# Kernel optimization log

Hardware: AMD Instinct MI355X
Metric: run time of the kernel (lower is better)

The kernel has to match this reference:

```python
import jax, jax.numpy as jnp
import numpy as np

NZ, NX, NY = 128, 256, 256
N_GAUSS = 50000
SIGMA_CUTOFF = 3.0
R = 3  # hardcoded stencil radius in voxelize()


def setup_inputs() -> dict:
    key = jax.random.key(0)
    k1, k2, k3, k4 = jax.random.split(key, 4)
    centers = jax.random.uniform(k1, (N_GAUSS, 3), jnp.float32) * 2.0 - 1.0
    log_scales = jnp.full((N_GAUSS, 3), -4.0, jnp.float32)
    rho_real = jax.random.normal(k2, (N_GAUSS,), jnp.float32) * 0.1
    rho_imag = jax.random.normal(k3, (N_GAUSS,), jnp.float32) * 0.1
    # k-space undersampling mask (0/1)
    mask = (jax.random.uniform(k4, (NZ, NX, NY), jnp.float32) < 0.3).astype(jnp.float32)
    return {"mask": mask, "centers": centers, "log_scales": log_scales,
            "rho_real": rho_real, "rho_imag": rho_imag}


def _voxelize(centers, log_scales, rho_real, rho_imag):
    gr = jnp.arange(-R, R + 1)
    kz, kx, ky = jnp.meshgrid(gr, gr, gr, indexing='ij')
    offsets = jnp.stack([kz, kx, ky], axis=-1).reshape(-1, 3)  # [K,3], K=343
    dims = jnp.array([NZ, NX, NY], jnp.int32)
    gsm1 = (dims - 1).astype(jnp.float32)  # grid_size - 1
    # nearest voxel of each gaussian center ([-1,1] -> grid coords)
    ci = jnp.round((centers + 1.0) * 0.5 * gsm1).astype(jnp.int32)  # [M,3]
    ni = ci[:, None, :] + offsets[None, :, :]                        # [M,K,3]
    in_bounds = jnp.all((ni >= 0) & (ni < dims), axis=-1)            # [M,K]
    # neighbor coords back in normalized [-1,1] space
    nc = ni.astype(jnp.float32) / gsm1 * 2.0 - 1.0                   # [M,K,3]
    scales = jnp.exp(log_scales)
    delta = (nc - centers[:, None, :]) / (scales[:, None, :] + 1e-8)
    dist_sq = jnp.sum(delta * delta, axis=-1)                        # [M,K]
    valid = in_bounds & (dist_sq <= SIGMA_CUTOFF ** 2)
    w = jnp.where(valid, jnp.exp(-0.5 * dist_sq), 0.0)               # [M,K]
    vals_r = (rho_real[:, None] * w).ravel()
    vals_i = (rho_imag[:, None] * w).ravel()
    # clip indices for safety; invalid entries contribute 0
    nic = jnp.clip(ni, 0, dims - 1)
    flat = ((nic[..., 0] * NX + nic[..., 1]) * NY + nic[..., 2]).ravel()
    vol_r = jnp.zeros(NZ * NX * NY, jnp.float32).at[flat].add(vals_r).reshape(NZ, NX, NY)
    vol_i = jnp.zeros(NZ * NX * NY, jnp.float32).at[flat].add(vals_i).reshape(NZ, NX, NY)
    return vol_r + 1j * vol_i


def _image_to_kspace(vol):
    # centered orthonormal 3D FFT (standard MRI convention)
    return jnp.fft.fftshift(jnp.fft.fftn(jnp.fft.ifftshift(vol), norm='ortho'))


def reference(mask, centers, log_scales, rho_real, rho_imag):
    volume = _voxelize(centers, log_scales, rho_real, rho_imag)
    kspace_pred = mask * _image_to_kspace(volume)
    return (volume, kspace_pred)
```

## Files before the change

### kernel.cpp

```cpp
#include <hip/hip_runtime.h>
#include <math.h>

#define NZd 128
#define NXd 256
#define NYd 256
#define NVOX (NZd * NXd * NYd)
#define PI_F 3.14159265358979323846f
#define SCALE_ORTHO 3.4526698300124393e-4f
#define CAP 512

__global__ void zero_kernel(float4* __restrict__ p, int n4) {
    int i = blockIdx.x * blockDim.x + threadIdx.x;
    if (i < n4) p[i] = make_float4(0.f, 0.f, 0.f, 0.f);
}
__global__ void zero_ints_kernel(int* __restrict__ p, int n) {
    int i = blockIdx.x * blockDim.x + threadIdx.x;
    if (i < n) p[i] = 0;
}

__global__ void voxelize_kernel(const float* __restrict__ centers,
                                const float* __restrict__ log_scales,
                                const float* __restrict__ rho_r,
                                const float* __restrict__ rho_i,
                                float* __restrict__ vol, int M) {
    long long t = (long long)blockIdx.x * blockDim.x + threadIdx.x;
    if (t >= (long long)M * 343) return;
    int g = (int)(t / 343);
    int k = (int)(t % 343);
    int oz = k / 49 - 3, ox = (k / 7) % 7 - 3, oy = k % 7 - 3;
    float cz = centers[g * 3 + 0], cx = centers[g * 3 + 1], cy = centers[g * 3 + 2];
    int iz = (int)rintf((cz + 1.0f) * 0.5f * 127.0f);
    int ix = (int)rintf((cx + 1.0f) * 0.5f * 255.0f);
    int iy = (int)rintf((cy + 1.0f) * 0.5f * 255.0f);
    int nz = iz + oz, nx = ix + ox, ny = iy + oy;
    if (nz < 0 || nz >= NZd || nx < 0 || nx >= NXd || ny < 0 || ny >= NYd) return;
    float sz = expf(log_scales[g * 3 + 0]) + 1e-8f;
    float sx = expf(log_scales[g * 3 + 1]) + 1e-8f;
    float sy = expf(log_scales[g * 3 + 2]) + 1e-8f;
    float dz = ((float)nz / 127.0f * 2.0f - 1.0f - cz) / sz;
    float dx = ((float)nx / 255.0f * 2.0f - 1.0f - cx) / sx;
    float dy = ((float)ny / 255.0f * 2.0f - 1.0f - cy) / sy;
    float d2 = dz * dz + dx * dx + dy * dy;
    if (d2 > 9.0f) return;
    float w = expf(-0.5f * d2);
    int idx = (nz * NXd + nx) * NYd + ny;
    atomicAdd(&vol[2 * idx + 0], rho_r[g] * w);
    atomicAdd(&vol[2 * idx + 1], rho_i[g] * w);
}

__global__ void copy_real_kernel(const float2* __restrict__ cvol,
                                 float* __restrict__ out) {
    int i = blockIdx.x * blockDim.x + threadIdx.x;
    out[i] = cvol[i].x;
}

__device__ __forceinline__ void center_voxel(const float* __restrict__ centers,
                                             int g, int& iz, int& ix, int& iy) {
    float cz = centers[g * 3 + 0], cx = centers[g * 3 + 1], cy = centers[g * 3 + 2];
    iz = min(max((int)rintf((cz + 1.0f) * 0.5f * 127.0f), 0), 127);
    ix = min(max((int)rintf((cx + 1.0f) * 0.5f * 255.0f), 0), 255);
    iy = min(max((int)rintf((cy + 1.0f) * 0.5f * 255.0f), 0), 255);
}

__global__ void bin_count_kernel(const float* __restrict__ centers,
                                 int* __restrict__ cnt, int M) {
    int g = blockIdx.x * blockDim.x + threadIdx.x;
    if (g >= M) return;
    int iz, ix, iy;
    center_voxel(centers, g, iz, ix, iy);
    atomicAdd(&cnt[((iz >> 4) << 8) | ((ix >> 4) << 4) | (iy >> 4)], 1);
}

__global__ void bin_scan_kernel(const int* __restrict__ cnt,
                                int* __restrict__ off,
                                int* __restrict__ cursor) {
    int lane = threadIdx.x;
    int base = lane << 5;
    int s = 0;
    #pragma unroll
    for (int i = 0; i < 32; i++) s += cnt[base + i];
    int incl = s;
    #pragma unroll
    for (int d = 1; d < 64; d <<= 1) {
        int v = __shfl_up(incl, d, 64);
        if (lane >= d) incl += v;
    }
    int run = incl - s;
    for (int i = 0; i < 32; i++) {
        int c = cnt[base + i];
        off[base + i] = run;
        cursor[base + i] = run;
        run += c;
    }
}

__global__ void bin_scatter_kernel(const float* __restrict__ centers,
                                   const float* __restrict__ log_scales,
                                   const float* __restrict__ rho_r,
                                   const float* __restrict__ rho_i,
                                   int* __restrict__ cursor,
                                   int* __restrict__ ciA,
                                   float* __restrict__ czA, float* __restrict__ cxA,
                                   float* __restrict__ cyA,
                                   float* __restrict__ iszA, float* __restrict__ isxA,
                                   float* __restrict__ isyA,
                                   float* __restrict__ rrA, float* __restrict__ riA,
                                   int M) {
    int g = blockIdx.x * blockDim.x + threadIdx.x;
    if (g >= M) return;
    int iz, ix, iy;
    center_voxel(centers, g, iz, ix, iy);
    int b = ((iz >> 4) << 8) | ((ix >> 4) << 4) | (iy >> 4);
    int pos = atomicAdd(&cursor[b], 1);
    ciA[pos] = (iz << 16) | (ix << 8) | iy;
    czA[pos] = centers[g * 3 + 0];
    cxA[pos] = centers[g * 3 + 1];
    cyA[pos] = centers[g * 3 + 2];
    iszA[pos] = 1.0f / (expf(log_scales[g * 3 + 0]) + 1e-8f);
    isxA[pos] = 1.0f / (expf(log_scales[g * 3 + 1]) + 1e-8f);
    isyA[pos] = 1.0f / (expf(log_scales[g * 3 + 2]) + 1e-8f);
    rrA[pos] = rho_r[g];
    riA[pos] = rho_i[g];
}

__global__ __launch_bounds__(256) void tile_accum_kernel(
        const int* __restrict__ cnt, const int* __restrict__ off,
        const int* __restrict__ ciA,
        const float* __restrict__ czA, const float* __restrict__ cxA,
        const float* __restrict__ cyA,
        const float* __restrict__ iszA, const float* __restrict__ isxA,
        const float* __restrict__ isyA,
        const float* __restrict__ rrA, const float* __restrict__ riA,
        float2* __restrict__ cvol, float* __restrict__ out_vr) {
    __shared__ int   sci[CAP];
    __shared__ float scz[CAP], scx[CAP], scy[CAP];
    __shared__ float sisz[CAP], sisx[CAP], sisy[CAP];
    __shared__ float srr[CAP], sri[CAP];
    __shared__ int wcnt[4];

    int tile = blockIdx.x;
    int ty = tile & 15, tx = (tile >> 4) & 15, tz = tile >> 8;
    int z0 = tz << 3, x0 = tx << 4, y0 = ty << 4;
    int t = threadIdx.x;
    int lane = t & 63, wid = t >> 6;
    int yl = t & 15, xl = t >> 4;
    int nx = x0 + xl, ny = y0 + yl;
    float nxf = (float)nx * (2.0f / 255.0f) - 1.0f;
    float nyf = (float)ny * (2.0f / 255.0f) - 1.0f;

    float accR[8], accI[8], zfs[8];
    #pragma unroll
    for (int i = 0; i < 8; i++) {
        accR[i] = 0.f; accI[i] = 0.f;
        zfs[i] = (float)(z0 + i) * (2.0f / 127.0f) - 1.0f;
    }

    int bzl = max(z0 - 3, 0) >> 4,  bzh = min(z0 + 10, 127) >> 4;
    int bxl = max(x0 - 3, 0) >> 4,  bxh = min(x0 + 18, 255) >> 4;
    int byl = max(y0 - 3, 0) >> 4,  byh = min(y0 + 18, 255) >> 4;

#define MKRANGE(slot, BZ, BX, VALID)                                          \
    int qs##slot = 0, len##slot = 0;                                          \
    if (VALID) {                                                              \
        int bl_ = ((BZ) << 8) | ((BX) << 4) | byl;                            \
        int bh_ = ((BZ) << 8) | ((BX) << 4) | byh;                            \
        qs##slot = off[bl_];                                                  \
        len##slot = off[bh_] + cnt[bh_] - qs##slot;                           \
    }
    bool hz1 = (bzh > bzl);
    bool hx1 = (bxh >= bxl + 1), hx2 = (bxh >= bxl + 2);
    MKRANGE(0, bzl,     bxl,     true)
    MKRANGE(1, bzl,     bxl + 1, hx1)
    MKRANGE(2, bzl,     bxl + 2, hx2)
    MKRANGE(3, bzl + 1, bxl,     hz1)
    MKRANGE(4, bzl + 1, bxl + 1, hz1 && hx1)
    MKRANGE(5, bzl + 1, bxl + 2, hz1 && hx2)
#undef MKRANGE
    int cum1 = len0;
    int cum2 = cum1 + len1;
    int cum3 = cum2 + len2;
    int cum4 = cum3 + len3;
    int cum5 = cum4 + len4;
    int T    = cum5 + len5;

    int lc = 0;
    for (int f0 = 0; f0 < T; f0 += 256) {
        int f = f0 + t;
        bool keep = false;
        int cpv = 0;
        float czv, cxv, cyv, iszv, isxv, isyv, rrv, riv;
        if (f < T) {
            int q = qs0 + f;
            if (f >= cum1) q = qs1 + (f - cum1);
            if (f >= cum2) q = qs2 + (f - cum2);
            if (f >= cum3) q = qs3 + (f - cum3);
            if (f >= cum4) q = qs4 + (f - cum4);
            if (f >= cum5) q = qs5 + (f - cum5);
            cpv = ciA[q];
            int iz = cpv >> 16, ix = (cpv >> 8) & 255, iy = cpv & 255;
            keep = !(ix + 3 < x0 || ix > x0 + 18 ||
                     iy + 3 < y0 || iy > y0 + 18 ||
                     iz + 3 < z0 || iz > z0 + 10);
            if (keep) {
                czv = czA[q]; cxv = cxA[q]; cyv = cyA[q];
                iszv = iszA[q]; isxv = isxA[q]; isyv = isyA[q];
                rrv = rrA[q]; riv = riA[q];
            }
        }
        unsigned long long m = __ballot(keep);
        __syncthreads();
        if (lane == 0) wcnt[wid] = __popcll(m);
        __syncthreads();
        int ntot = wcnt[0] + wcnt[1] + wcnt[2] + wcnt[3];
        if (lc + ntot > CAP) {
            for (int u = 0; u < lc; u++) {
                int cp = sci[u];
                int iz = cp >> 16, ix = (cp >> 8) & 255, iy = cp & 255;
                int dxi = nx - ix, dyi = ny - iy;
                if (dxi < -3 || dxi > 3 || dyi < -3 || dyi > 3) continue;
                float dxv = (nxf - scx[u]) * sisx[u];
                float dyv = (nyf - scy[u]) * sisy[u];
                float dxy2 = dxv * dxv + dyv * dyv;
                if (dxy2 > 9.0f) continue;
                float cz_ = scz[u], isz_ = sisz[u];
                float rr = srr[u], ri = sri[u];
                int zlo = max(z0, iz - 3) - z0;
                int zhi = min(z0 + 7, iz + 3) - z0;
                #pragma unroll
                for (int zl = 0; zl < 8; zl++) {
                    if (zl >= zlo && zl <= zhi) {
                        float dzv = (zfs[zl] - cz_) * isz_;
                        float d2 = dxy2 + dzv * dzv;
                        if (d2 <= 9.0f) {
                            float w = __expf(-0.5f * d2);
                            accR[zl] += rr * w;
                            accI[zl] += ri * w;
                        }
                    }
                }
            }
            __syncthreads();
            lc = 0;
        }
        int basew = lc;
        #pragma unroll
        for (int w = 0; w < 4; w++) if (w < wid) basew += wcnt[w];
        if (keep) {
            int pos = basew + __popcll(m & ((1ULL << lane) - 1));
            sci[pos] = cpv;
            scz[pos] = czv; scx[pos] = cxv; scy[pos] = cyv;
            sisz[pos] = iszv; sisx[pos] = isxv; sisy[pos] = isyv;
            srr[pos] = rrv; sri[pos] = riv;
        }
        lc += ntot;
    }
    __syncthreads();
    for (int u = 0; u < lc; u++) {
        int cp = sci[u];
        int iz = cp >> 16, ix = (cp >> 8) & 255, iy = cp & 255;
        int dxi = nx - ix, dyi = ny - iy;
        if (dxi < -3 || dxi > 3 || dyi < -3 || dyi > 3) continue;
        float dxv = (nxf - scx[u]) * sisx[u];
        float dyv = (nyf - scy[u]) * sisy[u];
        float dxy2 = dxv * dxv + dyv * dyv;
        if (dxy2 > 9.0f) continue;
        float cz_ = scz[u], isz_ = sisz[u];
        float rr = srr[u], ri = sri[u];
        int zlo = max(z0, iz - 3) - z0;
        int zhi = min(z0 + 7, iz + 3) - z0;
        #pragma unroll
        for (int zl = 0; zl < 8; zl++) {
            if (zl >= zlo && zl <= zhi) {
                float dzv = (zfs[zl] - cz_) * isz_;
                float d2 = dxy2 + dzv * dzv;
                if (d2 <= 9.0f) {
                    float w = __expf(-0.5f * d2);
                    accR[zl] += rr * w;
                    accI[zl] += ri * w;
                }
            }
        }
    }

    #pragma unroll
    for (int zl = 0; zl < 8; zl++) {
        size_t idx = ((size_t)(z0 + zl) * NXd + nx) * NYd + ny;
        cvol[idx] = make_float2(accR[zl], accI[zl]);
        out_vr[idx] = accR[zl];
    }
}

template <int L>
__device__ __forceinline__ void fft_lds(float2* buf) {
    int tid = threadIdx.x;
    for (int half = 1; half < L; half <<= 1) {
        __syncthreads();
        int j = tid & (half - 1);
        int i0 = ((tid ^ j) << 1) | j;
        int i1 = i0 + half;
        float ang = -PI_F * (float)j / (float)half;
        float s, c;
        sincosf(ang, &s, &c);
        float2 a = buf[i0];
        float2 b = buf[i1];
        float tr = c * b.x - s * b.y;
        float ti = c * b.y + s * b.x;
        buf[i0] = make_float2(a.x + tr, a.y + ti);
        buf[i1] = make_float2(a.x - tr, a.y - ti);
    }
    __syncthreads();
}

__global__ void fft_y_kernel(const float2* __restrict__ src,
                             float2* __restrict__ dst) {
    __shared__ float2 buf[256];
    __shared__ float2 tw[128];
    int l = blockIdx.x;
    int tid = threadIdx.x;
    {
        float s, c;
        sincosf(-PI_F * (float)tid / 128.0f, &s, &c);
        tw[tid] = make_float2(c, s);
    }
    int p = ((l >> 8) + l) & 1;
    const float2* s = src + (size_t)l * NYd;
    for (int i = tid; i < 256; i += 128) {
        float2 v = s[i];
        if ((p + i) & 1) { v.x = -v.x; v.y = -v.y; }
        buf[__brev((unsigned)i) >> 24] = v;
    }
    #pragma unroll
    for (int st = 0; st < 8; st++) {
        const int half = 1 << st;
        const int twstep = 128 >> st;
        __syncthreads();
        int j = tid & (half - 1);
        int i0 = ((tid ^ j) << 1) | j;
        int i1 = i0 + half;
        float2 w = tw[j * twstep];
        float2 a = buf[i0];
        float2 b = buf[i1];
        float tr = w.x * b.x - w.y * b.y;
        float ti = w.x * b.y + w.y * b.x;
        buf[i0] = make_float2(a.x + tr, a.y + ti);
        buf[i1] = make_float2(a.x - tr, a.y - ti);
    }
    __syncthreads();
    float2* d = dst + (size_t)l * NYd;
    for (int i = tid; i < 256; i += 128) d[i] = buf[i];
}

__global__ void fft_x_kernel(float2* __restrict__ ks) {
    __shared__ float2 buf[256];
    int l = blockIdx.x;
    int tid = threadIdx.x;
    int z = l >> 8, y = l & 255;
    float2* base = ks + (size_t)z * (NXd * NYd) + y;
    for (int i = tid; i < 256; i += 128)
        buf[__brev((unsigned)i) >> 24] = base[(size_t)i * NYd];
    fft_lds<256>(buf);
    for (int i = tid; i < 256; i += 128)
        base[(size_t)i * NYd] = buf[i];
}
__global__ void fft_z_kernel(float2* __restrict__ ks,
                             const float* __restrict__ mask,
                             float* __restrict__ out_real) {
    __shared__ float2 buf[128];
    int l = blockIdx.x;
    int tid = threadIdx.x;
    float2* base = ks + l;
    for (int i = tid; i < 128; i += 64)
        buf[__brev((unsigned)i) >> 25] = base[(size_t)i * (NXd * NYd)];
    fft_lds<128>(buf);
    int p = ((l >> 8) + l) & 1;
    for (int i = tid; i < 128; i += 64) {
        float2 v = buf[i];
        float sgn = ((p + i) & 1) ? -SCALE_ORTHO : SCALE_ORTHO;
        float m = mask[(size_t)i * (NXd * NYd) + l] * sgn;
        if (out_real) {
            out_real[(size_t)i * (NXd * NYd) + l] = v.x * m;
        } else {
            v.x *= m; v.y *= m;
            base[(size_t)i * (NXd * NYd)] = v;
        }
    }
}

__global__ __launch_bounds__(256) void fft_x16_kernel(float2* __restrict__ ks) {
    __shared__ float2 buf[16][256 + 1];
    __shared__ float2 tw[128];
    int t = threadIdx.x;
    int blk = blockIdx.x;
    int z = blk >> 4;
    int y16 = (blk & 15) << 4;
    if (t < 128) {
        float s, c;
        sincosf(-PI_F * (float)t / 128.0f, &s, &c);
        tw[t] = make_float2(c, s);
    }
    float2* base = ks + (size_t)z * (NXd * NYd) + y16;
    int yl = t & 15, xe0 = t >> 4;
    #pragma unroll
    for (int p = 0; p < 16; p++) {
        int xe = xe0 + (p << 4);
        float2 v = base[(size_t)xe * NYd + yl];
        buf[yl][__brev((unsigned)xe) >> 24] = v;
    }
    int s_ = t & 127;
    int fb0 = t >> 7;
    #pragma unroll
    for (int st = 0; st < 8; st++) {
        const int half = 1 << st;
        const int twstep = 128 >> st;
        __syncthreads();
        int j = s_ & (half - 1);
        int i0 = ((s_ ^ j) << 1) | j;
        int i1 = i0 + half;
        float2 w = tw[j * twstep];
        #pragma unroll
        for (int u = 0; u < 8; u++) {
            int fb = fb0 + (u << 1);
            float2 a = buf[fb][i0];
            float2 b = buf[fb][i1];
            float tr = w.x * b.x - w.y * b.y;
            float ti = w.x * b.y + w.y * b.x;
            buf[fb][i0] = make_float2(a.x + tr, a.y + ti);
            buf[fb][i1] = make_float2(a.x - tr, a.y - ti);
        }
    }
    __syncthreads();
    #pragma unroll
    for (int p = 0; p < 16; p++) {
        int xe = xe0 + (p << 4);
        base[(size_t)xe * NYd + yl] = buf[yl][xe];
    }
}

__global__ __launch_bounds__(256) void fft_z32_kernel(const float2* __restrict__ ks,
                                                      const float* __restrict__ mask,
                                                      float* __restrict__ out_kr) {
    __shared__ float2 buf[32][128 + 1];
    __shared__ float2 tw[64];
    int t = threadIdx.x;
    int blk = blockIdx.x;
    int kx = blk >> 3;
    int ky32 = (blk & 7) << 5;
    if (t < 64) {
        float s, c;
        sincosf(-PI_F * (float)t / 64.0f, &s, &c);
        tw[t] = make_float2(c, s);
    }
    const float2* base = ks + (size_t)kx * NYd + ky32;
    int kyl = t & 31, ze0 = t >> 5;
    #pragma unroll
    for (int p = 0; p < 16; p++) {
        int ze = ze0 + (p << 3);
        float2 v = base[(size_t)ze * (NXd * NYd) + kyl];
        buf[kyl][__brev((unsigned)ze) >> 25] = v;
    }
    int s_ = t & 63;
    int fb0 = t >> 6;
    #pragma unroll
    for (int st = 0; st < 7; st++) {
        const int half = 1 << st;
        const int twstep = 64 >> st;
        __syncthreads();
        int j = s_ & (half - 1);
        int i0 = ((s_ ^ j) << 1) | j;
        int i1 = i0 + half;
        float2 w = tw[j * twstep];
        #pragma unroll
        for (int u = 0; u < 8; u++) {
            int fb = fb0 + (u << 2);
            float2 a = buf[fb][i0];
            float2 b = buf[fb][i1];
            float tr = w.x * b.x - w.y * b.y;
            float ti = w.x * b.y + w.y * b.x;
            buf[fb][i0] = make_float2(a.x + tr, a.y + ti);
            buf[fb][i1] = make_float2(a.x - tr, a.y - ti);
        }
    }
    __syncthreads();
    int ky = ky32 + kyl;
    #pragma unroll
    for (int p = 0; p < 16; p++) {
        int ze = ze0 + (p << 3);
        float2 v = buf[kyl][ze];
        size_t gi = (size_t)ze * (NXd * NYd) + (size_t)kx * NYd + ky;
        float sgn = ((ze + kx + ky) & 1) ? -SCALE_ORTHO : SCALE_ORTHO;
        out_kr[gi] = v.x * (mask[gi] * sgn);
    }
}

extern "C" void kernel_launch(void* const* d_in, const int* in_sizes, int n_in,
                              void* d_out, int out_size, void* d_ws, size_t ws_size,
                              hipStream_t stream) {
    const float* mask       = (const float*)d_in[0];
    const float* centers    = (const float*)d_in[1];
    const float* log_scales = (const float*)d_in[2];
    const float* rho_r      = (const float*)d_in[3];
    const float* rho_i      = (const float*)d_in[4];
    int M = in_sizes[1] / 3;

    bool inter = (out_size >= 4 * NVOX);
    if (!inter) {
        if (out_size < 2 * NVOX || ws_size < (size_t)NVOX * 8) {
            int z4 = out_size / 4;
            if (z4 > 0)
                zero_kernel<<<(z4 + 255) / 256, 256, 0, stream>>>((float4*)d_out, z4);
            return;
        }
        float* out_vr = (float*)d_out;
        float* out_kr = out_vr + NVOX;
        float2* cvol = (float2*)d_ws;

        int Mpad = (M + 63) & ~63;
        bool fast = (8192 + 9LL * Mpad) <= (long long)NVOX;
        if (fast) {
            int* ibase  = (int*)out_kr;
            int* cnt    = ibase;
            int* off    = ibase + 2048;
            int* cursor = ibase + 4096;
            float* fbase = (float*)(ibase + 8192);
            int*   ciA  = (int*)fbase;
            float* czA  = fbase + 1LL * Mpad;
            float* cxA  = fbase + 2LL * Mpad;
            float* cyA  = fbase + 3LL * Mpad;
            float* iszA = fbase + 4LL * Mpad;
            float* isxA = fbase + 5LL * Mpad;
            float* isyA = fbase + 6LL * Mpad;
            float* rrA  = fbase + 7LL * Mpad;
            float* riA  = fbase + 8LL * Mpad;

            zero_ints_kernel<<<8, 256, 0, stream>>>(cnt, 2048);
            bin_count_kernel<<<(M + 255) / 256, 256, 0, stream>>>(centers, cnt, M);
            bin_scan_kernel<<<1, 64, 0, stream>>>(cnt, off, cursor);
            bin_scatter_kernel<<<(M + 255) / 256, 256, 0, stream>>>(
                centers, log_scales, rho_r, rho_i, cursor,
                ciA, czA, cxA, cyA, iszA, isxA, isyA, rrA, riA, M);
            tile_accum_kernel<<<4096, 256, 0, stream>>>(
                cnt, off, ciA, czA, cxA, cyA, iszA, isxA, isyA, rrA, riA,
                cvol, out_vr);
        } else {
            int n4 = (2 * NVOX) / 4;
            zero_kernel<<<(n4 + 255) / 256, 256, 0, stream>>>((float4*)cvol, n4);
            long long total = (long long)M * 343;
            int vb = (int)((total + 255) / 256);
            voxelize_kernel<<<vb, 256, 0, stream>>>(centers, log_scales, rho_r,
                                                    rho_i, (float*)cvol, M);
            copy_real_kernel<<<NVOX / 256, 256, 0, stream>>>(cvol, out_vr);
        }

        fft_y_kernel<<<NZd * NXd, 128, 0, stream>>>(cvol, cvol);
        fft_x16_kernel<<<NZd * 16, 256, 0, stream>>>(cvol);
        fft_z32_kernel<<<NXd * 8, 256, 0, stream>>>(cvol, mask, out_kr);
    } else {
        float2* cvol = (float2*)d_out;
        float2* cks  = cvol + NVOX;
        int n4 = (2 * NVOX) / 4;
        zero_kernel<<<(n4 + 255) / 256, 256, 0, stream>>>((float4*)cvol, n4);
        long long total = (long long)M * 343;
        int vb = (int)((total + 255) / 256);
        voxelize_kernel<<<vb, 256, 0, stream>>>(centers, log_scales, rho_r,
                                                rho_i, (float*)cvol, M);
        fft_y_kernel<<<NZd * NXd, 128, 0, stream>>>(cvol, cks);
        fft_x_kernel<<<NZd * NYd, 128, 0, stream>>>(cks);
        fft_z_kernel<<<NXd * NYd, 64, 0, stream>>>(cks, mask, nullptr);
    }
}
```

Baseline: 196.9 us.

## Pack tile-accum LDS into float4s, add per-wave x culling, batch FFT-y rows

After: 199.6 us. No clear change (+1.4%).

```diff
diff --git a/kernel.cpp b/kernel.cpp
--- a/kernel.cpp
+++ b/kernel.cpp
@@ -12,10 +12,6 @@
 __global__ void zero_kernel(float4* __restrict__ p, int n4) {
     int i = blockIdx.x * blockDim.x + threadIdx.x;
     if (i < n4) p[i] = make_float4(0.f, 0.f, 0.f, 0.f);
-}
-__global__ void zero_ints_kernel(int* __restrict__ p, int n) {
-    int i = blockIdx.x * blockDim.x + threadIdx.x;
-    if (i < n) p[i] = 0;
 }
 
 __global__ void voxelize_kernel(const float* __restrict__ centers,
@@ -132,10 +128,9 @@
         const float* __restrict__ isyA,
         const float* __restrict__ rrA, const float* __restrict__ riA,
         float2* __restrict__ cvol, float* __restrict__ out_vr) {
-    __shared__ int   sci[CAP];
-    __shared__ float scz[CAP], scx[CAP], scy[CAP];
-    __shared__ float sisz[CAP], sisx[CAP], sisy[CAP];
-    __shared__ float srr[CAP], sri[CAP];
+    __shared__ int    sci[CAP];
+    __shared__ float4 srA[CAP];
+    __shared__ float4 srB[CAP];
     __shared__ int wcnt[4];
 
     int tile = blockIdx.x;
@@ -147,6 +142,8 @@
     int nx = x0 + xl, ny = y0 + yl;
     float nxf = (float)nx * (2.0f / 255.0f) - 1.0f;
     float nyf = (float)ny * (2.0f / 255.0f) - 1.0f;
+    int wxlo = x0 + (wid << 2);
+    int wxhi = wxlo + 3;
 
     float accR[8], accI[8], zfs[8];
     #pragma unroll
@@ -182,6 +179,36 @@
     int cum4 = cum3 + len3;
     int cum5 = cum4 + len4;
     int T    = cum5 + len5;
+
+#define PROCESS_LIST()                                                        \
+    for (int u = 0; u < lc; u++) {                                            \
+        int cp = sci[u];                                                      \
+        int ix = (cp >> 8) & 255;                                             \
+        if (ix + 3 < wxlo || ix - 3 > wxhi) continue;       \
+        int iz = cp >> 16, iy = cp & 255;                                     \
+        int dxi = nx - ix, dyi = ny - iy;                                     \
+        bool colok = (dxi >= -3 && dxi <= 3 && dyi >= -3 && dyi <= 3);        \
+        float4 rA = srA[u];                                                   \
+        float dxv = (nxf - rA.x) * rA.z;                                      \
+        float dyv = (nyf - rA.y) * rA.w;                                      \
+        float dxy2 = dxv * dxv + dyv * dyv;                                   \
+        if (!colok || dxy2 > 9.0f) continue;                                  \
+        float4 rB = srB[u];                                                   \
+        int zlo = max(z0, iz - 3) - z0;                                       \
+        int zhi = min(z0 + 7, iz + 3) - z0;                                   \
+        _Pragma("unroll")                                                     \
+        for (int zl = 0; zl < 8; zl++) {                                      \
+            if (zl >= zlo && zl <= zhi) {                                     \
+                float dzv = (zfs[zl] - rB.x) * rB.y;                          \
+                float d2 = dxy2 + dzv * dzv;                                  \
+                if (d2 <= 9.0f) {                                             \
+                    float w = __expf(-0.5f * d2);                             \
+                    accR[zl] += rB.z * w;                                     \
+                    accI[zl] += rB.w * w;                                     \
+                }                                                             \
+            }                                                                 \
+        }                                                                     \
+    }
 
     int lc = 0;
     for (int f0 = 0; f0 < T; f0 += 256) {
@@ -213,32 +240,7 @@
         __syncthreads();
         int ntot = wcnt[0] + wcnt[1] + wcnt[2] + wcnt[3];
         if (lc + ntot > CAP) {
-            for (int u = 0; u < lc; u++) {
-                int cp = sci[u];
-                int iz = cp >> 16, ix = (cp >> 8) & 255, iy = cp & 255;
-                int dxi = nx - ix, dyi = ny - iy;
-                if (dxi < -3 || dxi > 3 || dyi < -3 || dyi > 3) continue;
-                float dxv = (nxf - scx[u]) * sisx[u];
-                float dyv = (nyf - scy[u]) * sisy[u];
-                float dxy2 = dxv * dxv + dyv * dyv;
-                if (dxy2 > 9.0f) continue;
-                float cz_ = scz[u], isz_ = sisz[u];
-                float rr = srr[u], ri = sri[u];
-                int zlo = max(z0, iz - 3) - z0;
-                int zhi = min(z0 + 7, iz + 3) - z0;
-                #pragma unroll
-                for (int zl = 0; zl < 8; zl++) {
-                    if (zl >= zlo && zl <= zhi) {
-                        float dzv = (zfs[zl] - cz_) * isz_;
-                        float d2 = dxy2 + dzv * dzv;
-                        if (d2 <= 9.0f) {
-                            float w = __expf(-0.5f * d2);
-                            accR[zl] += rr * w;
-                            accI[zl] += ri * w;
-                        }
-                    }
-                }
-            }
+            PROCESS_LIST()
             __syncthreads();
             lc = 0;
         }
@@ -248,39 +250,14 @@
         if (keep) {
             int pos = basew + __popcll(m & ((1ULL << lane) - 1));
             sci[pos] = cpv;
-            scz[pos] = czv; scx[pos] = cxv; scy[pos] = cyv;
-            sisz[pos] = iszv; sisx[pos] = isxv; sisy[pos] = isyv;
-            srr[pos] = rrv; sri[pos] = riv;
+            srA[pos] = make_float4(cxv, cyv, isxv, isyv);
+            srB[pos] = make_float4(czv, iszv, rrv, riv);
         }
         lc += ntot;
     }
     __syncthreads();
-    for (int u = 0; u < lc; u++) {
-        int cp = sci[u];
-        int iz = cp >> 16, ix = (cp >> 8) & 255, iy = cp & 255;
-        int dxi = nx - ix, dyi = ny - iy;
-        if (dxi < -3 || dxi > 3 || dyi < -3 || dyi > 3) continue;
-        float dxv = (nxf - scx[u]) * sisx[u];
-        float dyv = (nyf - scy[u]) * sisy[u];
-        float dxy2 = dxv * dxv + dyv * dyv;
-        if (dxy2 > 9.0f) continue;
-        float cz_ = scz[u], isz_ = sisz[u];
-        float rr = srr[u], ri = sri[u];
-        int zlo = max(z0, iz - 3) - z0;
-        int zhi = min(z0 + 7, iz + 3) - z0;
-        #pragma unroll
-        for (int zl = 0; zl < 8; zl++) {
-            if (zl >= zlo && zl <= zhi) {
-                float dzv = (zfs[zl] - cz_) * isz_;
-                float d2 = dxy2 + dzv * dzv;
-                if (d2 <= 9.0f) {
-                    float w = __expf(-0.5f * d2);
-                    accR[zl] += rr * w;
-                    accI[zl] += ri * w;
-                }
-            }
-        }
-    }
+    PROCESS_LIST()
+#undef PROCESS_LIST
 
     #pragma unroll
     for (int zl = 0; zl < 8; zl++) {
@@ -311,23 +288,25 @@
     __syncthreads();
 }
 
-__global__ void fft_y_kernel(const float2* __restrict__ src,
-                             float2* __restrict__ dst) {
-    __shared__ float2 buf[256];
+__global__ __launch_bounds__(256) void fft_y2_kernel(const float2* __restrict__ src,
+                                                     float2* __restrict__ dst) {
+    __shared__ float2 buf[2][256];
     __shared__ float2 tw[128];
-    int l = blockIdx.x;
-    int tid = threadIdx.x;
-    {
+    int t = threadIdx.x;
+    int li = t >> 7;
+    int tid = t & 127;
+    int l = (blockIdx.x << 1) + li;
+    if (t < 128) {
         float s, c;
-        sincosf(-PI_F * (float)tid / 128.0f, &s, &c);
-        tw[tid] = make_float2(c, s);
+        sincosf(-PI_F * (float)t / 128.0f, &s, &c);
+        tw[t] = make_float2(c, s);
     }
     int p = ((l >> 8) + l) & 1;
     const float2* s = src + (size_t)l * NYd;
     for (int i = tid; i < 256; i += 128) {
         float2 v = s[i];
         if ((p + i) & 1) { v.x = -v.x; v.y = -v.y; }
-        buf[__brev((unsigned)i) >> 24] = v;
+        buf[li][__brev((unsigned)i) >> 24] = v;
     }
     #pragma unroll
     for (int st = 0; st < 8; st++) {
@@ -338,18 +317,34 @@
         int i0 = ((tid ^ j) << 1) | j;
         int i1 = i0 + half;
         float2 w = tw[j * twstep];
-        float2 a = buf[i0];
-        float2 b = buf[i1];
+        float2 a = buf[li][i0];
+        float2 b = buf[li][i1];
         float tr = w.x * b.x - w.y * b.y;
         float ti = w.x * b.y + w.y * b.x;
-        buf[i0] = make_float2(a.x + tr, a.y + ti);
-        buf[i1] = make_float2(a.x - tr, a.y - ti);
+        buf[li][i0] = make_float2(a.x + tr, a.y + ti);
+        buf[li][i1] = make_float2(a.x - tr, a.y - ti);
     }
     __syncthreads();
     float2* d = dst + (size_t)l * NYd;
+    for (int i = tid; i < 256; i += 128) d[i] = buf[li][i];
+}
+
+__global__ void fft_y_kernel(const float2* __restrict__ src,
+                             float2* __restrict__ dst) {
+    __shared__ float2 buf[256];
+    int l = blockIdx.x;
+    int tid = threadIdx.x;
+    int p = ((l >> 8) + l) & 1;
+    const float2* s = src + (size_t)l * NYd;
+    for (int i = tid; i < 256; i += 128) {
+        float2 v = s[i];
+        if ((p + i) & 1) { v.x = -v.x; v.y = -v.y; }
+        buf[__brev((unsigned)i) >> 24] = v;
+    }
+    fft_lds<256>(buf);
+    float2* d = dst + (size_t)l * NYd;
     for (int i = tid; i < 256; i += 128) d[i] = buf[i];
 }
-
 __global__ void fft_x_kernel(float2* __restrict__ ks) {
     __shared__ float2 buf[256];
     int l = blockIdx.x;
@@ -532,7 +527,7 @@
             float* rrA  = fbase + 7LL * Mpad;
             float* riA  = fbase + 8LL * Mpad;
 
-            zero_ints_kernel<<<8, 256, 0, stream>>>(cnt, 2048);
+            hipMemsetAsync(cnt, 0, 2048 * sizeof(int), stream);
             bin_count_kernel<<<(M + 255) / 256, 256, 0, stream>>>(centers, cnt, M);
             bin_scan_kernel<<<1, 64, 0, stream>>>(cnt, off, cursor);
             bin_scatter_kernel<<<(M + 255) / 256, 256, 0, stream>>>(
@@ -551,7 +546,7 @@
             copy_real_kernel<<<NVOX / 256, 256, 0, stream>>>(cvol, out_vr);
         }
 
-        fft_y_kernel<<<NZd * NXd, 128, 0, stream>>>(cvol, cvol);
+        fft_y2_kernel<<<NZd * NXd / 2, 256, 0, stream>>>(cvol, cvol);
         fft_x16_kernel<<<NZd * 16, 256, 0, stream>>>(cvol);
         fft_z32_kernel<<<NXd * 8, 256, 0, stream>>>(cvol, mask, out_kr);
     } else {
```
